# Optimization experiments

Hardware: AMD Instinct MI355X
Metric: run time of the kernel (lower is better)

Reference implementation:

```python
import jax, jax.numpy as jnp
import numpy as np

N_NODES = 50000
N_EDGES = 800000
D_IN = 256
D_OUT = 256
BN_EPS = 1e-5


def setup_inputs() -> dict:
    key = jax.random.key(0)
    k1, k2, k3 = jax.random.split(key, 3)
    x = jax.random.normal(k1, (N_NODES, D_IN), dtype=jnp.float32)
    edge_index = jax.random.randint(k2, (2, N_EDGES), 0, N_NODES, dtype=jnp.int64)
    # GCNConv linear weight [out, in] (glorot-ish scale), separate bias
    W = jax.random.normal(k3, (D_OUT, D_IN), dtype=jnp.float32) * (1.0 / np.sqrt(D_IN))
    bias = jnp.zeros((D_OUT,), dtype=jnp.float32)
    gamma = jnp.ones((D_OUT,), dtype=jnp.float32)
    beta = jnp.zeros((D_OUT,), dtype=jnp.float32)
    return {"x": x, "edge_index": edge_index, "W": W, "bias": bias, "gamma": gamma, "beta": beta}


def reference(x, edge_index, W, bias, gamma, beta):
    N = x.shape[0]
    self_loops = jnp.arange(N, dtype=edge_index.dtype)
    row = jnp.concatenate([edge_index[0], self_loops])  # source nodes
    col = jnp.concatenate([edge_index[1], self_loops])  # target nodes

    # linear transform first (PyG GCNConv order): [N, D_out]
    h = x @ W.T

    # symmetric degree normalization with self-loops
    deg = jax.ops.segment_sum(jnp.ones_like(col, dtype=h.dtype), col, num_segments=N)
    dinv = jnp.where(deg > 0, jax.lax.rsqrt(deg), 0.0)
    norm = dinv[row] * dinv[col]  # [E+N]

    # gather -> scale -> scatter-add
    msg = h[row] * norm[:, None]                         # [E+N, D_out]
    agg = jax.ops.segment_sum(msg, col, num_segments=N)  # [N, D_out]
    agg = agg + bias

    # BatchNorm (training mode: batch stats over nodes, biased var)
    mean = jnp.mean(agg, axis=0)
    var = jnp.mean((agg - mean) ** 2, axis=0)
    y = gamma * (agg - mean) * jax.lax.rsqrt(var + BN_EPS) + beta
    return jax.nn.relu(y)
```

## Files before the change

### kernel.cpp

```cpp
#include <hip/hip_runtime.h>
#include <cstdio>

#define NN 50000
#define NE 800000
#define DD 256
#define WS_NEED 113080000UL

__attribute__((constructor)) static void r19_on_load(void) {
    fprintf(stderr, "R19SO_LOADED\n");
    fflush(stderr);
}

__device__ float b2f(unsigned short u) {
    union { unsigned int i; float f; } c;
    c.i = ((unsigned int)u) << 16;
    return c.f;
}
__device__ float clampf(float v) { return fminf(fmaxf(v, -65504.f), 65504.f); }
__device__ float rdF(const void* p, long long idx, int ff) {
    if (ff) return clampf(b2f(((const unsigned short*)p)[idx]));
    return clampf(((const float*)p)[idx]);
}
__device__ unsigned short f2b_rne(float f) {
    union { float f; unsigned int u; } c;
    c.f = f;
    unsigned int r = (c.u + 0x7FFFu + ((c.u >> 16) & 1u)) >> 16;
    return (unsigned short)r;
}

typedef __attribute__((ext_vector_type(8))) short bf16x8;
typedef __attribute__((ext_vector_type(4))) float f32x4;
typedef __attribute__((ext_vector_type(4))) _Float16 f16x4;
typedef __attribute__((ext_vector_type(8))) _Float16 f16x8;

__global__ void g_zero(int* deg, float* sums, const unsigned short* xr,
                       const int* ei, int* flags) {
    if (blockIdx.x == 196) {
        __shared__ int acc[2];
        if (threadIdx.x < 2) acc[threadIdx.x] = 0;
        __syncthreads();
        int g = 0;
        for (int j = 0; j < 4; j++) {
            unsigned short u = xr[(threadIdx.x * 4 + j) * 2];
            int e = (u >> 7) & 0xFF;
            if (u == 0 || u == 0x8000 || (e >= 100 && e <= 140)) g++;
        }
        atomicAdd(&acc[0], g);
        if (ei[2 * threadIdx.x + 1] != 0) atomicAdd(&acc[1], 1);
        __syncthreads();
        if (threadIdx.x == 0) {
            flags[0] = (acc[0] >= 922) ? 1 : 0;
            flags[1] = (acc[1] == 0) ? 1 : 0;
        }
        return;
    }
    int i = blockIdx.x * 256 + threadIdx.x;
    if (i < NN) deg[i] = 0;
    if (i < 2 * DD) sums[i] = 0.f;
}

__global__ void g_cvt_ed(const int* raw, const int* flags, int* e32, int* deg) {
    int e = blockIdx.x * 256 + threadIdx.x;
    if (e >= NE) return;
    int f = flags[1];
    int r = f ? raw[2 * e] : raw[e];
    int c = f ? raw[2 * (NE + e)] : raw[NE + e];
    e32[e] = r;
    e32[NE + e] = c;
    if ((unsigned int)r < NN && (unsigned int)c < NN) atomicAdd(&deg[c], 1);
}

__global__ void g_cvt_w(const void* W, const void* bias, const void* gamma,
                        const void* beta, const int* flags, unsigned short* Wb,
                        float* pf) {
    int ff = flags[0];
    int t = threadIdx.x;
    if (blockIdx.x == 256) {
        pf[t] = rdF(bias, t, ff);
        pf[DD + t] = rdF(gamma, t, ff);
        pf[2 * DD + t] = rdF(beta, t, ff);
        return;
    }
    int i = blockIdx.x * 256 + t;
    Wb[i] = f2b_rne(rdF(W, i, ff));
}

__global__ __launch_bounds__(256) void g_scan1(const int* deg, int* off, int* bsum,
                                               float* dinv) {
    __shared__ int sm[256];
    int tid = threadIdx.x;
    int i = blockIdx.x * 256 + tid;
    int v = (i < NN) ? deg[i] : 0;
    sm[tid] = v;
    __syncthreads();
    for (int s = 1; s < 256; s <<= 1) {
        int t = (tid >= s) ? sm[tid - s] : 0;
        __syncthreads();
        sm[tid] += t;
        __syncthreads();
    }
    if (i < NN) {
        off[i] = sm[tid] - v;
        dinv[i] = rsqrtf((float)(v + 1));
    }
    if (tid == 255) bsum[blockIdx.x] = sm[255];
}

__global__ __launch_bounds__(256) void g_scan2(const int* bsum, int* bbase) {
    __shared__ int sm[256];
    int tid = threadIdx.x;
    int v = (tid < 196) ? bsum[tid] : 0;
    sm[tid] = v;
    __syncthreads();
    for (int s = 1; s < 256; s <<= 1) {
        int t = (tid >= s) ? sm[tid - s] : 0;
        __syncthreads();
        sm[tid] += t;
        __syncthreads();
    }
    if (tid < 196) bbase[tid] = sm[tid] - v;
}

__global__ void g_scan3(int* off, const int* bbase, int* cursor) {
    int i = blockIdx.x * 256 + threadIdx.x;
    if (i < NN) {
        int o = off[i] + bbase[i >> 8];
        off[i] = o;
        cursor[i] = o;
    }
}

#define WP 264
__global__ __launch_bounds__(256) void g_gemm_mfma(const void* x, const int* flags,
                                                   const unsigned short* Wb,
                                                   const float* dinv, _Float16* h) {
    __shared__ unsigned short wlds[64 * WP];
    int t = threadIdx.x;
    int rt = blockIdx.x >> 2;
    int ctile = blockIdx.x & 3;

    const unsigned short* wsrc = Wb + ctile * 64 * DD;
#pragma unroll
    for (int i = 0; i < 8; i++) {
        int c = t + i * 256;
        int row = c >> 5;
        int off = (c & 31) * 8;
        bf16x8 v = *(const bf16x8*)(wsrc + row * DD + off);
        *(bf16x8*)(&wlds[row * WP + off]) = v;
    }
    __syncthreads();

    int wave = t >> 6;
    int lane = t & 63;
    int rw = rt * 4 + wave;
    if (rw >= 3125) return;
    int r0 = rw * 16;
    int l15 = lane & 15;
    int kq = lane >> 4;

    bf16x8 a[8];
    int ff = flags[0];
    if (ff) {
        const unsigned short* p =
            (const unsigned short*)x + (unsigned long long)(r0 + l15) * DD + kq * 8;
#pragma unroll
        for (int k = 0; k < 8; k++)
            a[k] = *(const bf16x8*)(p + k * 32);
    } else {
        const float* p = (const float*)x + (unsigned long long)(r0 + l15) * DD + kq * 8;
#pragma unroll
        for (int k = 0; k < 8; k++) {
#pragma unroll
            for (int j = 0; j < 8; j++)
                a[k][j] = (short)f2b_rne(p[k * 32 + j]);
        }
    }

    float dv[4];
#pragma unroll
    for (int j = 0; j < 4; j++) dv[j] = dinv[r0 + kq * 4 + j];

    f32x4 acc[4];
#pragma unroll
    for (int ct = 0; ct < 4; ct++) acc[ct] = (f32x4){0.f, 0.f, 0.f, 0.f};

#pragma unroll
    for (int k = 0; k < 8; k++) {
        bf16x8 bfr[4];
#pragma unroll
        for (int ct = 0; ct < 4; ct++)
            bfr[ct] = *(const bf16x8*)(&wlds[(ct * 16 + l15) * WP + kq * 8 + k * 32]);
#pragma unroll
        for (int ct = 0; ct < 4; ct++)
            acc[ct] = __builtin_amdgcn_mfma_f32_16x16x32_bf16(a[k], bfr[ct], acc[ct],
                                                              0, 0, 0);
    }

#pragma unroll
    for (int ct = 0; ct < 4; ct++) {
        _Float16* op = h + (unsigned long long)(r0 + kq * 4) * DD + ctile * 64 +
                       ct * 16 + l15;
#pragma unroll
        for (int j = 0; j < 4; j++)
            op[(unsigned long long)j * DD] = (_Float16)(acc[ct][j] * dv[j]);
    }
}

__global__ void g_fill(const int* erow, const int* ecol, int* cursor, int* csrc) {
    int e = blockIdx.x * 256 + threadIdx.x;
    if (e < NE) {
        unsigned int c = (unsigned int)ecol[e];
        unsigned int r = (unsigned int)erow[e];
        if (c < NN && r < NN) {
            int slot = atomicAdd(&cursor[c], 1);
            if ((unsigned int)slot < NE) csrc[slot] = (int)r;
        }
    }
}

__global__ __launch_bounds__(256) void g_agg(const _Float16* h, const float* dinv,
                                             const int* off, const int* deg,
                                             const int* csrc, const float* pf,
                                             _Float16* agg) {
    int lane = threadIdx.x & 63;
    int n = blockIdx.x * 4 + (threadIdx.x >> 6);
    int f0 = lane * 4;
    int s = __builtin_amdgcn_readfirstlane(off[n]);
    int cnt = __builtin_amdgcn_readfirstlane(deg[n]);
    float dn = dinv[n];
    f16x4 hv = *(const f16x4*)(h + (unsigned long long)n * DD + f0);
    float a0 = (float)hv[0];
    float a1 = (float)hv[1];
    float a2 = (float)hv[2];
    float a3 = (float)hv[3];
    const int* ip = csrc + s;
    int k = 0;
    for (; k + 8 <= cnt; k += 8) {
        int i0 = ip[k + 0], i1 = ip[k + 1], i2 = ip[k + 2], i3 = ip[k + 3];
        int i4 = ip[k + 4], i5 = ip[k + 5], i6 = ip[k + 6], i7 = ip[k + 7];
        f16x4 v0 = *(const f16x4*)(h + (unsigned long long)i0 * DD + f0);
        f16x4 v1 = *(const f16x4*)(h + (unsigned long long)i1 * DD + f0);
        f16x4 v2 = *(const f16x4*)(h + (unsigned long long)i2 * DD + f0);
        f16x4 v3 = *(const f16x4*)(h + (unsigned long long)i3 * DD + f0);
        f16x4 v4 = *(const f16x4*)(h + (unsigned long long)i4 * DD + f0);
        f16x4 v5 = *(const f16x4*)(h + (unsigned long long)i5 * DD + f0);
        f16x4 v6 = *(const f16x4*)(h + (unsigned long long)i6 * DD + f0);
        f16x4 v7 = *(const f16x4*)(h + (unsigned long long)i7 * DD + f0);
        a0 += (((float)v0[0] + (float)v1[0]) + ((float)v2[0] + (float)v3[0])) +
              (((float)v4[0] + (float)v5[0]) + ((float)v6[0] + (float)v7[0]));
        a1 += (((float)v0[1] + (float)v1[1]) + ((float)v2[1] + (float)v3[1])) +
              (((float)v4[1] + (float)v5[1]) + ((float)v6[1] + (float)v7[1]));
        a2 += (((float)v0[2] + (float)v1[2]) + ((float)v2[2] + (float)v3[2])) +
              (((float)v4[2] + (float)v5[2]) + ((float)v6[2] + (float)v7[2]));
        a3 += (((float)v0[3] + (float)v1[3]) + ((float)v2[3] + (float)v3[3])) +
              (((float)v4[3] + (float)v5[3]) + ((float)v6[3] + (float)v7[3]));
    }
    for (; k + 4 <= cnt; k += 4) {
        int i0 = ip[k + 0], i1 = ip[k + 1], i2 = ip[k + 2], i3 = ip[k + 3];
        f16x4 v0 = *(const f16x4*)(h + (unsigned long long)i0 * DD + f0);
        f16x4 v1 = *(const f16x4*)(h + (unsigned long long)i1 * DD + f0);
        f16x4 v2 = *(const f16x4*)(h + (unsigned long long)i2 * DD + f0);
        f16x4 v3 = *(const f16x4*)(h + (unsigned long long)i3 * DD + f0);
        a0 += ((float)v0[0] + (float)v1[0]) + ((float)v2[0] + (float)v3[0]);
        a1 += ((float)v0[1] + (float)v1[1]) + ((float)v2[1] + (float)v3[1]);
        a2 += ((float)v0[2] + (float)v1[2]) + ((float)v2[2] + (float)v3[2]);
        a3 += ((float)v0[3] + (float)v1[3]) + ((float)v2[3] + (float)v3[3]);
    }
    for (; k < cnt; k++) {
        int i0 = ip[k];
        f16x4 v0 = *(const f16x4*)(h + (unsigned long long)i0 * DD + f0);
        a0 += (float)v0[0];
        a1 += (float)v0[1];
        a2 += (float)v0[2];
        a3 += (float)v0[3];
    }
    f16x4 o;
    o[0] = (_Float16)(dn * a0 + pf[f0 + 0]);
    o[1] = (_Float16)(dn * a1 + pf[f0 + 1]);
    o[2] = (_Float16)(dn * a2 + pf[f0 + 2]);
    o[3] = (_Float16)(dn * a3 + pf[f0 + 3]);
    *(f16x4*)(agg + (unsigned long long)n * DD + f0) = o;
}

__global__ __launch_bounds__(256) void g_stats(const _Float16* agg, float* sums) {
    int t = threadIdx.x;
    float s = 0.f;
    float s2 = 0.f;
    for (int n = blockIdx.x; n < NN; n += 256) {
        float v = (float)agg[(unsigned long long)n * DD + t];
        s += v;
        s2 += v * v;
    }
    atomicAdd(&sums[t], s);
    atomicAdd(&sums[DD + t], s2);
}

__global__ void g_fin(const float* sums, const float* pf, float* ss) {
    int t = threadIdx.x;
    float mean = sums[t] * (1.0f / NN);
    float var = sums[DD + t] * (1.0f / NN) - mean * mean;
    var = fmaxf(var, 0.f);
    float sc = pf[DD + t] * rsqrtf(var + 1e-5f);
    ss[t] = sc;
    ss[DD + t] = pf[2 * DD + t] - mean * sc;
}

__global__ void DenseGCNLayer_2937757631000_kernel(const _Float16* agg, const float* ss,
                                                   float* out) {
    int t = threadIdx.x;
    unsigned long long base =
        (unsigned long long)blockIdx.x * 2048 + (unsigned int)t * 8;
    int f = (int)(base & 255);
    f16x8 v = *(const f16x8*)(agg + base);
    f32x4 o0, o1;
#pragma unroll
    for (int j = 0; j < 4; j++)
        o0[j] = fmaxf(ss[f + j] * (float)v[j] + ss[DD + f + j], 0.f);
#pragma unroll
    for (int j = 0; j < 4; j++)
        o1[j] = fmaxf(ss[f + 4 + j] * (float)v[4 + j] + ss[DD + f + 4 + j], 0.f);
    *(f32x4*)(out + base) = o0;
    *(f32x4*)(out + base + 4) = o1;
}

extern "C" void kernel_launch(void* const* d_in, const int* in_sizes, int n_in,
                              void* d_out, int out_size, void* d_ws, size_t ws_size,
                              hipStream_t stream) {
    const void* x = d_in[0];
    const int* ei = (const int*)d_in[1];
    const void* W = d_in[2];
    const void* bias = d_in[3];
    const void* gamma = d_in[4];
    const void* beta = d_in[5];
    char* ws = (char*)d_ws;
    float* out = (float*)d_out;

    _Float16* h = (_Float16*)(ws + 0UL);
    _Float16* agg = (_Float16*)(ws + 51200000UL);
    int* e32 = (int*)(ws + 102400000UL);
    int* csrc = (int*)(ws + 108800000UL);
    unsigned short* Wb = (unsigned short*)(ws + 112000000UL);
    int* deg = (int*)(ws + 112262144UL);
    float* dinv = (float*)(ws + 112462336UL);
    int* off = (int*)(ws + 112662528UL);
    int* cursor = (int*)(ws + 112862720UL);
    int* bsum = (int*)(ws + 113062912UL);
    int* bbase = (int*)(ws + 113063936UL);
    float* pf = (float*)(ws + 113064960UL);
    float* sums = (float*)(ws + 113068032UL);
    float* ss = (float*)(ws + 113070080UL);
    int* flags = (int*)(ws + 113072128UL);
    const int* erow = e32;
    const int* ecol = e32 + NE;

    if (ws_size < WS_NEED) {
        fprintf(stderr, "R19_WS_SMALL %zu\n", ws_size);
        fflush(stderr);
        return;
    }

    g_zero<<<197, 256, 0, stream>>>(deg, sums, (const unsigned short*)x, ei, flags);
    g_cvt_ed<<<3125, 256, 0, stream>>>(ei, flags, e32, deg);
    g_cvt_w<<<257, 256, 0, stream>>>(W, bias, gamma, beta, flags, Wb, pf);
    g_scan1<<<196, 256, 0, stream>>>(deg, off, bsum, dinv);
    g_scan2<<<1, 256, 0, stream>>>(bsum, bbase);
    g_scan3<<<196, 256, 0, stream>>>(off, bbase, cursor);
    g_gemm_mfma<<<3128, 256, 0, stream>>>(x, flags, Wb, dinv, h);
    g_fill<<<3125, 256, 0, stream>>>(erow, ecol, cursor, csrc);
    g_agg<<<12500, 256, 0, stream>>>(h, dinv, off, deg, csrc, pf, agg);
    g_stats<<<256, 256, 0, stream>>>(agg, sums);
    g_fin<<<1, 256, 0, stream>>>(sums, pf, ss);
    DenseGCNLayer_2937757631000_kernel<<<6250, 256, 0, stream>>>(agg, ss, out);
}
```

Before: 347.5 us.

## Fuse setup, scan, gemm+fill and stats kernels to cut launch count

Merges zeroing, flag detection and weight/param conversion into one setup kernel, with each weight-conversion block re-detecting the dtype flag locally. The three-pass prefix scan is replaced by a single pass in which each block claims its CSR segment base with a global atomic. The CSR fill runs as extra blocks of the GEMM launch so the two overlap, and BN finalisation moves into the last-finishing stats block. The aim is to remove launch gaps and serial tiny kernels. In exchange, the CSR segments are ordered nondeterministically and the code now relies on atomic and fence correctness for the last-block finalisation.

New measurement: 366.7 us. +5.5%, slower.

```diff
diff --git a/kernel.cpp b/kernel.cpp
--- a/kernel.cpp
+++ b/kernel.cpp
@@ -6,8 +6,8 @@
 #define DD 256
 #define WS_NEED 113080000UL
 
-__attribute__((constructor)) static void r19_on_load(void) {
-    fprintf(stderr, "R19SO_LOADED\n");
+__attribute__((constructor)) static void r20_on_load(void) {
+    fprintf(stderr, "R20SO_LOADED\n");
     fflush(stderr);
 }
 
@@ -33,33 +33,55 @@
 typedef __attribute__((ext_vector_type(4))) _Float16 f16x4;
 typedef __attribute__((ext_vector_type(8))) _Float16 f16x8;
 
-__global__ void g_zero(int* deg, float* sums, const unsigned short* xr,
-                       const int* ei, int* flags) {
-    if (blockIdx.x == 196) {
-        __shared__ int acc[2];
-        if (threadIdx.x < 2) acc[threadIdx.x] = 0;
+__device__ int detect_ff(const unsigned short* xr) {
+    __shared__ int dacc;
+    if (threadIdx.x == 0) dacc = 0;
+    __syncthreads();
+    int g = 0;
+    for (int j = 0; j < 4; j++) {
+        unsigned short u = xr[(threadIdx.x * 4 + j) * 2];
+        int e = (u >> 7) & 0xFF;
+        if (u == 0 || u == 0x8000 || (e >= 100 && e <= 140)) g++;
+    }
+    atomicAdd(&dacc, g);
+    __syncthreads();
+    return dacc >= 922;
+}
+
+__global__ void k_setup(int* deg, float* sums, int* misc, const unsigned short* xr,
+                        const int* ei, int* flags, const void* W, const void* bias,
+                        const void* gamma, const void* beta, unsigned short* Wb,
+                        float* pf) {
+    int b = blockIdx.x;
+    int t = threadIdx.x;
+    if (b < 196) {
+        int i = b * 256 + t;
+        if (i < NN) deg[i] = 0;
+        if (i < 2 * DD) sums[i] = 0.f;
+        if (i < 16) misc[i] = 0;
+        return;
+    }
+    if (b == 196) {
+        __shared__ int acc2;
+        if (t == 0) acc2 = 0;
+        int ff = detect_ff(xr);
+        if (ei[2 * t + 1] != 0) atomicAdd(&acc2, 1);
         __syncthreads();
-        int g = 0;
-        for (int j = 0; j < 4; j++) {
-            unsigned short u = xr[(threadIdx.x * 4 + j) * 2];
-            int e = (u >> 7) & 0xFF;
-            if (u == 0 || u == 0x8000 || (e >= 100 && e <= 140)) g++;
+        if (t == 0) {
+            flags[0] = ff;
+            flags[1] = (acc2 == 0) ? 1 : 0;
         }
-        atomicAdd(&acc[0], g);
-        if (ei[2 * threadIdx.x + 1] != 0) atomicAdd(&acc[1], 1);
-        __syncthreads();
-        if (threadIdx.x == 0) {
-            flags[0] = (acc[0] >= 922) ? 1 : 0;
-            flags[1] = (acc[1] == 0) ? 1 : 0;
-        }
+        pf[t] = rdF(bias, t, ff);
+        pf[DD + t] = rdF(gamma, t, ff);
+        pf[2 * DD + t] = rdF(beta, t, ff);
         return;
     }
-    int i = blockIdx.x * 256 + threadIdx.x;
-    if (i < NN) deg[i] = 0;
-    if (i < 2 * DD) sums[i] = 0.f;
-}
-
-__global__ void g_cvt_ed(const int* raw, const int* flags, int* e32, int* deg) {
+    int ff = detect_ff(xr);
+    int i = (b - 197) * 256 + t;
+    Wb[i] = f2b_rne(rdF(W, i, ff));
+}
+
+__global__ void k_edges(const int* raw, const int* flags, int* e32, int* deg) {
     int e = blockIdx.x * 256 + threadIdx.x;
     if (e >= NE) return;
     int f = flags[1];
@@ -70,24 +92,10 @@
     if ((unsigned int)r < NN && (unsigned int)c < NN) atomicAdd(&deg[c], 1);
 }
 
-__global__ void g_cvt_w(const void* W, const void* bias, const void* gamma,
-                        const void* beta, const int* flags, unsigned short* Wb,
-                        float* pf) {
-    int ff = flags[0];
-    int t = threadIdx.x;
-    if (blockIdx.x == 256) {
-        pf[t] = rdF(bias, t, ff);
-        pf[DD + t] = rdF(gamma, t, ff);
-        pf[2 * DD + t] = rdF(beta, t, ff);
-        return;
-    }
-    int i = blockIdx.x * 256 + t;
-    Wb[i] = f2b_rne(rdF(W, i, ff));
-}
-
-__global__ __launch_bounds__(256) void g_scan1(const int* deg, int* off, int* bsum,
-                                               float* dinv) {
+__global__ __launch_bounds__(256) void k_alloc(const int* deg, int* off, int* cursor,
+                                               float* dinv, int* gcur) {
     __shared__ int sm[256];
+    __shared__ int sbase;
     int tid = threadIdx.x;
     int i = blockIdx.x * 256 + tid;
     int v = (i < NN) ? deg[i] : 0;
@@ -99,41 +107,34 @@
         sm[tid] += t;
         __syncthreads();
     }
+    if (tid == 255) sbase = atomicAdd(gcur, sm[255]);
+    __syncthreads();
     if (i < NN) {
-        off[i] = sm[tid] - v;
-        dinv[i] = rsqrtf((float)(v + 1));
-    }
-    if (tid == 255) bsum[blockIdx.x] = sm[255];
-}
-
-__global__ __launch_bounds__(256) void g_scan2(const int* bsum, int* bbase) {
-    __shared__ int sm[256];
-    int tid = threadIdx.x;
-    int v = (tid < 196) ? bsum[tid] : 0;
-    sm[tid] = v;
-    __syncthreads();
-    for (int s = 1; s < 256; s <<= 1) {
-        int t = (tid >= s) ? sm[tid - s] : 0;
-        __syncthreads();
-        sm[tid] += t;
-        __syncthreads();
-    }
-    if (tid < 196) bbase[tid] = sm[tid] - v;
-}
-
-__global__ void g_scan3(int* off, const int* bbase, int* cursor) {
-    int i = blockIdx.x * 256 + threadIdx.x;
-    if (i < NN) {
-        int o = off[i] + bbase[i >> 8];
+        int o = sbase + sm[tid] - v;
         off[i] = o;
         cursor[i] = o;
+        dinv[i] = rsqrtf((float)(v + 1));
     }
 }
 
 #define WP 264
-__global__ __launch_bounds__(256) void g_gemm_mfma(const void* x, const int* flags,
-                                                   const unsigned short* Wb,
-                                                   const float* dinv, _Float16* h) {
+__global__ __launch_bounds__(256) void k_gf(const void* x, const int* flags,
+                                            const unsigned short* Wb,
+                                            const float* dinv, _Float16* h,
+                                            const int* erow, const int* ecol,
+                                            int* cursor, int* csrc) {
+    if (blockIdx.x >= 3128) {
+        int e = (blockIdx.x - 3128) * 256 + threadIdx.x;
+        if (e < NE) {
+            unsigned int c = (unsigned int)ecol[e];
+            unsigned int r = (unsigned int)erow[e];
+            if (c < NN && r < NN) {
+                int slot = atomicAdd(&cursor[c], 1);
+                if ((unsigned int)slot < NE) csrc[slot] = (int)r;
+            }
+        }
+        return;
+    }
     __shared__ unsigned short wlds[64 * WP];
     int t = threadIdx.x;
     int rt = blockIdx.x >> 2;
@@ -203,18 +204,6 @@
 #pragma unroll
         for (int j = 0; j < 4; j++)
             op[(unsigned long long)j * DD] = (_Float16)(acc[ct][j] * dv[j]);
-    }
-}
-
-__global__ void g_fill(const int* erow, const int* ecol, int* cursor, int* csrc) {
-    int e = blockIdx.x * 256 + threadIdx.x;
-    if (e < NE) {
-        unsigned int c = (unsigned int)ecol[e];
-        unsigned int r = (unsigned int)erow[e];
-        if (c < NN && r < NN) {
-            int slot = atomicAdd(&cursor[c], 1);
-            if ((unsigned int)slot < NE) csrc[slot] = (int)r;
-        }
     }
 }
 
@@ -282,7 +271,8 @@
     *(f16x4*)(agg + (unsigned long long)n * DD + f0) = o;
 }
 
-__global__ __launch_bounds__(256) void g_stats(const _Float16* agg, float* sums) {
+__global__ __launch_bounds__(256) void k_stats(const _Float16* agg, float* sums,
+                                               const float* pf, float* ss, int* done) {
     int t = threadIdx.x;
     float s = 0.f;
     float s2 = 0.f;
@@ -293,16 +283,22 @@
     }
     atomicAdd(&sums[t], s);
     atomicAdd(&sums[DD + t], s2);
-}
-
-__global__ void g_fin(const float* sums, const float* pf, float* ss) {
-    int t = threadIdx.x;
-    float mean = sums[t] * (1.0f / NN);
-    float var = sums[DD + t] * (1.0f / NN) - mean * mean;
-    var = fmaxf(var, 0.f);
-    float sc = pf[DD + t] * rsqrtf(var + 1e-5f);
-    ss[t] = sc;
-    ss[DD + t] = pf[2 * DD + t] - mean * sc;
+    __threadfence();
+    __syncthreads();
+    __shared__ int lastf;
+    if (t == 0) lastf = (atomicAdd(done, 1) == 255) ? 1 : 0;
+    __syncthreads();
+    if (lastf) {
+        float sv = __hip_atomic_load(&sums[t], __ATOMIC_RELAXED,
+                                     __HIP_MEMORY_SCOPE_AGENT);
+        float sv2 = __hip_atomic_load(&sums[DD + t], __ATOMIC_RELAXED,
+                                      __HIP_MEMORY_SCOPE_AGENT);
+        float mean = sv * (1.0f / NN);
+        float var = fmaxf(sv2 * (1.0f / NN) - mean * mean, 0.f);
+        float sc = pf[DD + t] * rsqrtf(var + 1e-5f);
+        ss[t] = sc;
+        ss[DD + t] = pf[2 * DD + t] - mean * sc;
+    }
 }
 
 __global__ void DenseGCNLayer_2937757631000_kernel(const _Float16* agg, const float* ss,
@@ -344,8 +340,7 @@
     float* dinv = (float*)(ws + 112462336UL);
     int* off = (int*)(ws + 112662528UL);
     int* cursor = (int*)(ws + 112862720UL);
-    int* bsum = (int*)(ws + 113062912UL);
-    int* bbase = (int*)(ws + 113063936UL);
+    int* misc = (int*)(ws + 113063936UL);
     float* pf = (float*)(ws + 113064960UL);
     float* sums = (float*)(ws + 113068032UL);
     float* ss = (float*)(ws + 113070080UL);
@@ -354,21 +349,17 @@
     const int* ecol = e32 + NE;
 
     if (ws_size < WS_NEED) {
-        fprintf(stderr, "R19_WS_SMALL %zu\n", ws_size);
+        fprintf(stderr, "R20_WS_SMALL %zu\n", ws_size);
         fflush(stderr);
         return;
     }
 
-    g_zero<<<197, 256, 0, stream>>>(deg, sums, (const unsigned short*)x, ei, flags);
-    g_cvt_ed<<<3125, 256, 0, stream>>>(ei, flags, e32, deg);
-    g_cvt_w<<<257, 256, 0, stream>>>(W, bias, gamma, beta, flags, Wb, pf);
-    g_scan1<<<196, 256, 0, stream>>>(deg, off, bsum, dinv);
-    g_scan2<<<1, 256, 0, stream>>>(bsum, bbase);
-    g_scan3<<<196, 256, 0, stream>>>(off, bbase, cursor);
-    g_gemm_mfma<<<3128, 256, 0, stream>>>(x, flags, Wb, dinv, h);
-    g_fill<<<3125, 256, 0, stream>>>(erow, ecol, cursor, csrc);
+    k_setup<<<453, 256, 0, stream>>>(deg, sums, misc, (const unsigned short*)x, ei,
+                                     flags, W, bias, gamma, beta, Wb, pf);
+    k_edges<<<3125, 256, 0, stream>>>(ei, flags, e32, deg);
+    k_alloc<<<196, 256, 0, stream>>>(deg, off, cursor, dinv, &misc[0]);
+    k_gf<<<6253, 256, 0, stream>>>(x, flags, Wb, dinv, h, erow, ecol, cursor, csrc);
     g_agg<<<12500, 256, 0, stream>>>(h, dinv, off, deg, csrc, pf, agg);
-    g_stats<<<256, 256, 0, stream>>>(agg, sums);
-    g_fin<<<1, 256, 0, stream>>>(sums, pf, ss);
+    k_stats<<<256, 256, 0, stream>>>(agg, sums, pf, ss, &misc[1]);
     DenseGCNLayer_2937757631000_kernel<<<6250, 256, 0, stream>>>(agg, ss, out);
 }
```
